# Kernel tuning notes

Hardware: AMD Instinct MI355X
Metric: run time of the kernel (lower is better)

The kernel has to match this reference:

```python
import jax, jax.numpy as jnp
import numpy as np

ALPHA = 0.95   # membrane decay
VTH = 1.0      # firing threshold
BN_EPS = 1e-5
SS_BETA = 10.0  # SuperSpike surrogate slope (used in bwd module)


def _spike(v):
    # Heaviside spike on (v - vth) already subtracted
    return (v > 0).astype(v.dtype)


def _batchnorm(h, scale, bias):
    # per-timestep batch norm over the batch axis (train mode, batch stats)
    mu = jnp.mean(h, axis=0, keepdims=True)
    var = jnp.mean(jnp.square(h - mu), axis=0, keepdims=True)
    return (h - mu) * jax.lax.rsqrt(var + BN_EPS) * scale + bias


def _lif_layer(x, W, scale=None, bias=None):
    # x: [T, B, F_in] -> spikes z: [T, B, F_out]
    T, B, _ = x.shape
    F_out = W.shape[1]
    I = jnp.einsum('tbf,fo->tbo', x, W)  # precompute dense projection for all steps

    def step(v, i_t):
        if scale is not None:
            i_t = _batchnorm(i_t, scale, bias)
        v = ALPHA * v + i_t
        z = _spike(v - VTH)
        v = v * (1.0 - z)  # reset-to-zero
        return v, z

    v0 = jnp.zeros((B, F_out), dtype=x.dtype)
    _, z = jax.lax.scan(step, v0, I)
    return z


def setup_inputs() -> dict:
    key = jax.random.key(0)
    k1, k2, k3 = jax.random.split(key, 3)
    B, T, H, Wd, C = 512, 100, 28, 28, 2
    inputs = jax.random.uniform(k1, (B, T, H, Wd, C), dtype=jnp.float32)
    trgt = jax.random.randint(k2, (B,), 0, 10)
    W1 = jax.random.normal(k3, (784, 100), dtype=jnp.float32) * (1.0 / np.sqrt(784))
    bn_scale = jnp.ones((100,), dtype=jnp.float32)
    bn_bias = jnp.zeros((100,), dtype=jnp.float32)
    W2 = jax.random.normal(jax.random.fold_in(key, 7), (100, 10), dtype=jnp.float32) * (1.0 / np.sqrt(100))
    return {"inputs": inputs, "trgt": trgt, "W1": W1, "bn_scale": bn_scale,
            "bn_bias": bn_bias, "W2": W2}


def reference(inputs, trgt, W1, bn_scale, bn_bias, W2):
    # inputs: [B, T, H, W, C]
    x = jnp.mean(inputs, axis=-1, keepdims=True)        # [B,T,H,W,1]
    x = jnp.swapaxes(x, 0, 1)                            # [T,B,H,W,1]
    x = jnp.reshape(x, (x.shape[0], x.shape[1], -1))     # [T,B,784]
    z1 = _lif_layer(x, W1, bn_scale, bn_bias)            # [T,B,100]
    z2 = _lif_layer(z1, W2)                              # [T,B,10]
    out = jnp.mean(z2, axis=0)                           # [B,10]
    return out
```

## Files before the change

### kernel.cpp

```cpp
#include <hip/hip_runtime.h>

#define T_STEPS 100
#define BATCH   512
#define FIN     784
#define O1      100
#define O2      10
#define KC1     28
#define NC1     (FIN / KC1)

typedef __attribute__((ext_vector_type(4))) double f64x4;

__global__ __launch_bounds__(64) void k0_probe(int* __restrict__ maps) {
  const int l = threadIdx.x;
  const f64x4 z = {0.0, 0.0, 0.0, 0.0};
  f64x4 pr = __builtin_amdgcn_mfma_f64_16x16x4f64((double)(l & 15), 0.25, z, 0, 0, 0);
  f64x4 pc = __builtin_amdgcn_mfma_f64_16x16x4f64(0.25, (double)(l & 15), z, 0, 0, 0);
#pragma unroll
  for (int r = 0; r < 4; ++r) {
    int rm = (int)(pr[r] + 0.5); rm = rm < 0 ? 0 : (rm > 15 ? 15 : rm);
    int cm = (int)(pc[r] + 0.5); cm = cm < 0 ? 0 : (cm > 15 ? 15 : cm);
    maps[l * 8 + r]     = rm;
    maps[l * 8 + 4 + r] = cm;
  }
}

__global__ __launch_bounds__(512, 6) void k1_mfma(const float* __restrict__ in,
                                                  const float* __restrict__ W1,
                                                  const int* __restrict__ maps,
                                                  double* __restrict__ I1T) {
  __shared__ double AI[KC1][66];
  __shared__ double WS[KC1][O1];
  const int tid = threadIdx.x;
  const int l   = tid & 63;
  const int w   = tid >> 6;
  const int wb  = w & 3;
  const int wo  = w >> 2;
  const int r16 = l & 15;
  const int q16 = l >> 4;
  const int b0  = (int)blockIdx.x * 64;
  const int t   = (int)blockIdx.y;

  const int4 rm = *reinterpret_cast<const int4*>(maps + l * 8);
  const int4 cm = *reinterpret_cast<const int4*>(maps + l * 8 + 4);

  bool iact[2]; int irow[2], iq[2]; const float* ibp[2];
#pragma unroll
  for (int p = 0; p < 2; ++p) {
    const int i = p * 512 + tid;
    iact[p] = (i < 896);
    irow[p] = iact[p] ? i / 14 : 0;
    iq[p]   = i - irow[p] * 14;
    ibp[p]  = in + ((size_t)(b0 + irow[p]) * T_STEPS + t) * (FIN * 2) + iq[p] * 4;
  }
  bool wact[3]; int wk[3], woh[3]; const float2* wbp[3];
#pragma unroll
  for (int p = 0; p < 3; ++p) {
    const int i = p * 512 + tid;
    wact[p] = (i < 1400);
    wk[p]   = wact[p] ? i / 50 : 0;
    woh[p]  = (i - wk[p] * 50) * 2;
    wbp[p]  = reinterpret_cast<const float2*>(W1) + ((size_t)wk[p] * O1 + woh[p]) / 2;
  }

  float4 ist[2];
  float2 wst[3];

#pragma unroll
  for (int p = 0; p < 2; ++p) if (iact[p]) ist[p] = *reinterpret_cast<const float4*>(ibp[p]);
#pragma unroll
  for (int p = 0; p < 3; ++p) if (wact[p]) wst[p] = wbp[p][0];

  f64x4 acc0 = {0.0, 0.0, 0.0, 0.0};
  f64x4 acc1 = {0.0, 0.0, 0.0, 0.0};
  f64x4 acc2 = {0.0, 0.0, 0.0, 0.0};
  f64x4 acc3 = {0.0, 0.0, 0.0, 0.0};

  for (int c = 0; c < NC1; ++c) {
    __syncthreads();
#pragma unroll
    for (int p = 0; p < 2; ++p)
      if (iact[p]) {
        AI[iq[p] * 2 + 0][irow[p]] = 0.5 * ((double)ist[p].x + (double)ist[p].y);
        AI[iq[p] * 2 + 1][irow[p]] = 0.5 * ((double)ist[p].z + (double)ist[p].w);
      }
#pragma unroll
    for (int p = 0; p < 3; ++p)
      if (wact[p]) {
        double2 wv; wv.x = (double)wst[p].x; wv.y = (double)wst[p].y;
        *reinterpret_cast<double2*>(&WS[wk[p]][woh[p]]) = wv;
      }
    if (c + 1 < NC1) {
#pragma unroll
      for (int p = 0; p < 2; ++p)
        if (iact[p]) ist[p] = *reinterpret_cast<const float4*>(ibp[p] + (c + 1) * 56);
#pragma unroll
      for (int p = 0; p < 3; ++p)
        if (wact[p]) wst[p] = wbp[p][(size_t)(c + 1) * (KC1 * O1 / 2)];
    }
    __syncthreads();
    if (wo == 0) {
#pragma unroll
      for (int q = 0; q < KC1 / 4; ++q) {
        const double bv = AI[q * 4 + q16][wb * 16 + r16];
        const double* wr = &WS[q * 4 + q16][r16];
        acc0 = __builtin_amdgcn_mfma_f64_16x16x4f64(wr[0],  bv, acc0, 0, 0, 0);
        acc1 = __builtin_amdgcn_mfma_f64_16x16x4f64(wr[16], bv, acc1, 0, 0, 0);
        acc2 = __builtin_amdgcn_mfma_f64_16x16x4f64(wr[32], bv, acc2, 0, 0, 0);
        acc3 = __builtin_amdgcn_mfma_f64_16x16x4f64(wr[48], bv, acc3, 0, 0, 0);
      }
    } else {
#pragma unroll
      for (int q = 0; q < KC1 / 4; ++q) {
        const double bv = AI[q * 4 + q16][wb * 16 + r16];
        const double* wr = &WS[q * 4 + q16][r16];
        acc0 = __builtin_amdgcn_mfma_f64_16x16x4f64(wr[64], bv, acc0, 0, 0, 0);
        acc1 = __builtin_amdgcn_mfma_f64_16x16x4f64(wr[80], bv, acc1, 0, 0, 0);
        acc2 = __builtin_amdgcn_mfma_f64_16x16x4f64(wr[84], bv, acc2, 0, 0, 0);
      }
    }
  }

  double* base = I1T + (size_t)t * O1 * BATCH + (b0 + wb * 16);
#define STORE_TILE(ACC, O0)                                          \
  {                                                                  \
    base[(size_t)((O0) + rm.x) * BATCH + cm.x] = (ACC)[0];           \
    base[(size_t)((O0) + rm.y) * BATCH + cm.y] = (ACC)[1];           \
    base[(size_t)((O0) + rm.z) * BATCH + cm.z] = (ACC)[2];           \
    base[(size_t)((O0) + rm.w) * BATCH + cm.w] = (ACC)[3];           \
  }
  if (wo == 0) {
    STORE_TILE(acc0, 0);
    STORE_TILE(acc1, 16);
    STORE_TILE(acc2, 32);
    STORE_TILE(acc3, 48);
  } else {
    STORE_TILE(acc0, 64);
    STORE_TILE(acc1, 80);
    STORE_TILE(acc2, 84);
  }
#undef STORE_TILE
}

__global__ __launch_bounds__(256) void k2_bnstats(const double* __restrict__ I1T,
                                                  double* __restrict__ mu,
                                                  double* __restrict__ rstd) {
  const int r    = blockIdx.x * 4 + (threadIdx.x >> 6);
  const int lane = threadIdx.x & 63;
  const double2* row2 = reinterpret_cast<const double2*>(I1T + (size_t)r * BATCH) + lane * 4;
  double v[8];
#pragma unroll
  for (int u = 0; u < 4; ++u) {
    double2 p = row2[u];
    v[2 * u] = p.x; v[2 * u + 1] = p.y;
  }
  double s = 0.0;
#pragma unroll
  for (int u = 0; u < 8; ++u) s += v[u];
#pragma unroll
  for (int m = 32; m >= 1; m >>= 1) s += __shfl_xor(s, m, 64);
  const double mean = s / 512.0;
  double q = 0.0;
#pragma unroll
  for (int u = 0; u < 8; ++u) { double d = v[u] - mean; q += d * d; }
#pragma unroll
  for (int m = 32; m >= 1; m >>= 1) q += __shfl_xor(q, m, 64);
  if (lane == 0) {
    mu[r]   = mean;
    rstd[r] = 1.0 / sqrt(q / 512.0 + 1e-5);
  }
}

__global__ __launch_bounds__(512) void k3_lif1(const double* __restrict__ I1T,
                                               const double* __restrict__ mu,
                                               const double* __restrict__ rstd,
                                               const float* __restrict__ scale,
                                               const float* __restrict__ bias,
                                               float* __restrict__ z1T) {
  const int o = blockIdx.x;
  const int b = threadIdx.x;
  const double sc = (double)scale[o], bs = (double)bias[o];
  double v = 0.0;
  for (int tc = 0; tc < T_STEPS; tc += 10) {
    double x[10], muv[10], rsv[10];
#pragma unroll
    for (int u = 0; u < 10; ++u) {
      const int t = tc + u;
      x[u]   = I1T[((size_t)t * O1 + o) * BATCH + b];
      muv[u] = mu[t * O1 + o];
      rsv[u] = rstd[t * O1 + o];
    }
#pragma unroll
    for (int u = 0; u < 10; ++u) {
      const double i = ((x[u] - muv[u]) * rsv[u]) * sc + bs;
      v = 0.95 * v + i;
      const bool z = (v > 1.0);
      z1T[((size_t)(tc + u) * O1 + o) * BATCH + b] = z ? 1.0f : 0.0f;
      if (z) v = 0.0;
    }
  }
}

__global__ __launch_bounds__(512) void k4_proj2(const float* __restrict__ z1T,
                                                const float* __restrict__ W2,
                                                double* __restrict__ I2) {
  __shared__ double W2_lds[O1 * O2];
  const int t = blockIdx.x;
  const int b = threadIdx.x;
  for (int i = threadIdx.x; i < O1 * O2; i += 512) W2_lds[i] = (double)W2[i];
  __syncthreads();
  double acc[O2];
#pragma unroll
  for (int j = 0; j < O2; ++j) acc[j] = 0.0;
  for (int o = 0; o < O1; ++o) {
    const double z = (double)z1T[((size_t)t * O1 + o) * BATCH + b];
#pragma unroll
    for (int j = 0; j < O2; ++j) acc[j] += z * W2_lds[o * O2 + j];
  }
#pragma unroll
  for (int j = 0; j < O2; ++j)
    I2[((size_t)t * O2 + j) * BATCH + b] = acc[j];
}

__global__ __launch_bounds__(512) void k5_lif2(const double* __restrict__ I2,
                                               float* __restrict__ out) {
  const int j = blockIdx.x;
  const int b = threadIdx.x;
  double v = 0.0;
  int cnt = 0;
  for (int tc = 0; tc < T_STEPS; tc += 10) {
    double x[10];
#pragma unroll
    for (int u = 0; u < 10; ++u)
      x[u] = I2[((size_t)(tc + u) * O2 + j) * BATCH + b];
#pragma unroll
    for (int u = 0; u < 10; ++u) {
      v = 0.95 * v + x[u];
      if (v > 1.0) { ++cnt; v = 0.0; }
    }
  }
  out[b * O2 + j] = (float)((double)cnt / 100.0);
}

extern "C" void kernel_launch(void* const* d_in, const int* in_sizes, int n_in,
                              void* d_out, int out_size, void* d_ws, size_t ws_size,
                              hipStream_t stream) {
  const float* in    = (const float*)d_in[0];
  const float* W1    = (const float*)d_in[2];
  const float* scale = (const float*)d_in[3];
  const float* bias  = (const float*)d_in[4];
  const float* W2    = (const float*)d_in[5];
  float* out = (float*)d_out;

  char* ws = (char*)d_ws;
  size_t off = 0;
  int*    maps = (int*)(ws + off);    off += 4096;
  double* I1T  = (double*)(ws + off); off += (size_t)T_STEPS * O1 * BATCH * sizeof(double);
  double* mu   = (double*)(ws + off); off += (size_t)T_STEPS * O1 * sizeof(double);
  double* rstd = (double*)(ws + off); off += (size_t)T_STEPS * O1 * sizeof(double);
  float*  z1T  = (float*)(ws + off);  off += (size_t)T_STEPS * O1 * BATCH * sizeof(float);
  double* I2   = (double*)(ws + off); off += (size_t)T_STEPS * O2 * BATCH * sizeof(double);

  k0_probe  <<<dim3(1), 64, 0, stream>>>(maps);
  k1_mfma   <<<dim3(BATCH / 64, T_STEPS), 512, 0, stream>>>(in, W1, maps, I1T);
  k2_bnstats<<<dim3(T_STEPS * O1 / 4), 256, 0, stream>>>(I1T, mu, rstd);
  k3_lif1   <<<dim3(O1), 512, 0, stream>>>(I1T, mu, rstd, scale, bias, z1T);
  k4_proj2  <<<dim3(T_STEPS), 512, 0, stream>>>(z1T, W2, I2);
  k5_lif2   <<<dim3(O2), 512, 0, stream>>>(I2, out);
}
```

Baseline: 256.8 us.

## Load W1 directly into registers, shrink k1 tiles, inline MFMA lane-map probe

The W1 shared-memory staging is removed. Each lane now loads the weight values its MFMA operands need straight from global memory (L2/L1 cached) into registers per chunk. The batch tile halves to 32 with 256-thread blocks, which doubles the grid, and the separate probe kernel that computed MFMA lane mappings is folded into k1 as per-lane MFMA calls. This cuts LDS traffic, syncs and one kernel launch, but adds uncached-pattern global weight loads that are issued synchronously each chunk rather than prefetched.

Result: slower. 266.8 us (+3.9%).

```diff
diff --git a/kernel.cpp b/kernel.cpp
--- a/kernel.cpp
+++ b/kernel.cpp
@@ -10,71 +10,51 @@
 
 typedef __attribute__((ext_vector_type(4))) double f64x4;
 
-__global__ __launch_bounds__(64) void k0_probe(int* __restrict__ maps) {
-  const int l = threadIdx.x;
-  const f64x4 z = {0.0, 0.0, 0.0, 0.0};
-  f64x4 pr = __builtin_amdgcn_mfma_f64_16x16x4f64((double)(l & 15), 0.25, z, 0, 0, 0);
-  f64x4 pc = __builtin_amdgcn_mfma_f64_16x16x4f64(0.25, (double)(l & 15), z, 0, 0, 0);
-#pragma unroll
-  for (int r = 0; r < 4; ++r) {
-    int rm = (int)(pr[r] + 0.5); rm = rm < 0 ? 0 : (rm > 15 ? 15 : rm);
-    int cm = (int)(pc[r] + 0.5); cm = cm < 0 ? 0 : (cm > 15 ? 15 : cm);
-    maps[l * 8 + r]     = rm;
-    maps[l * 8 + 4 + r] = cm;
-  }
-}
-
-__global__ __launch_bounds__(512, 6) void k1_mfma(const float* __restrict__ in,
+__global__ __launch_bounds__(256, 4) void k1_mfma(const float* __restrict__ in,
                                                   const float* __restrict__ W1,
-                                                  const int* __restrict__ maps,
                                                   double* __restrict__ I1T) {
-  __shared__ double AI[KC1][66];
-  __shared__ double WS[KC1][O1];
+  __shared__ double AI[KC1][34];
   const int tid = threadIdx.x;
   const int l   = tid & 63;
   const int w   = tid >> 6;
-  const int wb  = w & 3;
-  const int wo  = w >> 2;
+  const int wb  = w & 1;
+  const int wo  = w >> 1;
   const int r16 = l & 15;
   const int q16 = l >> 4;
-  const int b0  = (int)blockIdx.x * 64;
+  const int b0  = (int)blockIdx.x * 32;
   const int t   = (int)blockIdx.y;
 
-  const int4 rm = *reinterpret_cast<const int4*>(maps + l * 8);
-  const int4 cm = *reinterpret_cast<const int4*>(maps + l * 8 + 4);
-
   bool iact[2]; int irow[2], iq[2]; const float* ibp[2];
 #pragma unroll
   for (int p = 0; p < 2; ++p) {
-    const int i = p * 512 + tid;
-    iact[p] = (i < 896);
+    const int i = p * 256 + tid;
+    iact[p] = (i < 448);
     irow[p] = iact[p] ? i / 14 : 0;
     iq[p]   = i - irow[p] * 14;
     ibp[p]  = in + ((size_t)(b0 + irow[p]) * T_STEPS + t) * (FIN * 2) + iq[p] * 4;
   }
-  bool wact[3]; int wk[3], woh[3]; const float2* wbp[3];
-#pragma unroll
-  for (int p = 0; p < 3; ++p) {
-    const int i = p * 512 + tid;
-    wact[p] = (i < 1400);
-    wk[p]   = wact[p] ? i / 50 : 0;
-    woh[p]  = (i - wk[p] * 50) * 2;
-    wbp[p]  = reinterpret_cast<const float2*>(W1) + ((size_t)wk[p] * O1 + woh[p]) / 2;
-  }
 
   float4 ist[2];
-  float2 wst[3];
-
 #pragma unroll
   for (int p = 0; p < 2; ++p) if (iact[p]) ist[p] = *reinterpret_cast<const float4*>(ibp[p]);
-#pragma unroll
-  for (int p = 0; p < 3; ++p) if (wact[p]) wst[p] = wbp[p][0];
+
+  const f64x4 z = {0.0, 0.0, 0.0, 0.0};
+  f64x4 pr = __builtin_amdgcn_mfma_f64_16x16x4f64((double)r16, 0.25, z, 0, 0, 0);
+  f64x4 pc = __builtin_amdgcn_mfma_f64_16x16x4f64(0.25, (double)r16, z, 0, 0, 0);
+  int rmv[4], cmv[4];
+#pragma unroll
+  for (int r = 0; r < 4; ++r) {
+    int rm = (int)(pr[r] + 0.5); rmv[r] = rm < 0 ? 0 : (rm > 15 ? 15 : rm);
+    int cm = (int)(pc[r] + 0.5); cmv[r] = cm < 0 ? 0 : (cm > 15 ? 15 : cm);
+  }
 
   f64x4 acc0 = {0.0, 0.0, 0.0, 0.0};
   f64x4 acc1 = {0.0, 0.0, 0.0, 0.0};
   f64x4 acc2 = {0.0, 0.0, 0.0, 0.0};
   f64x4 acc3 = {0.0, 0.0, 0.0, 0.0};
 
+  const float* pW0 = W1 + (size_t)q16 * O1 + r16 + (wo ? 64 : 0);
+
   for (int c = 0; c < NC1; ++c) {
     __syncthreads();
 #pragma unroll
@@ -83,50 +63,57 @@
         AI[iq[p] * 2 + 0][irow[p]] = 0.5 * ((double)ist[p].x + (double)ist[p].y);
         AI[iq[p] * 2 + 1][irow[p]] = 0.5 * ((double)ist[p].z + (double)ist[p].w);
       }
-#pragma unroll
-    for (int p = 0; p < 3; ++p)
-      if (wact[p]) {
-        double2 wv; wv.x = (double)wst[p].x; wv.y = (double)wst[p].y;
-        *reinterpret_cast<double2*>(&WS[wk[p]][woh[p]]) = wv;
-      }
+    float wreg[7][4];
+    const float* pWc = pW0 + (size_t)c * (KC1 * O1);
+    if (wo == 0) {
+#pragma unroll
+      for (int q = 0; q < 7; ++q) {
+        wreg[q][0] = pWc[q * 400 +  0];
+        wreg[q][1] = pWc[q * 400 + 16];
+        wreg[q][2] = pWc[q * 400 + 32];
+        wreg[q][3] = pWc[q * 400 + 48];
+      }
+    } else {
+#pragma unroll
+      for (int q = 0; q < 7; ++q) {
+        wreg[q][0] = pWc[q * 400 +  0];
+        wreg[q][1] = pWc[q * 400 + 16];
+        wreg[q][2] = pWc[q * 400 + 20];
+      }
+    }
     if (c + 1 < NC1) {
 #pragma unroll
       for (int p = 0; p < 2; ++p)
         if (iact[p]) ist[p] = *reinterpret_cast<const float4*>(ibp[p] + (c + 1) * 56);
-#pragma unroll
-      for (int p = 0; p < 3; ++p)
-        if (wact[p]) wst[p] = wbp[p][(size_t)(c + 1) * (KC1 * O1 / 2)];
     }
     __syncthreads();
     if (wo == 0) {
 #pragma unroll
-      for (int q = 0; q < KC1 / 4; ++q) {
+      for (int q = 0; q < 7; ++q) {
         const double bv = AI[q * 4 + q16][wb * 16 + r16];
-        const double* wr = &WS[q * 4 + q16][r16];
-        acc0 = __builtin_amdgcn_mfma_f64_16x16x4f64(wr[0],  bv, acc0, 0, 0, 0);
-        acc1 = __builtin_amdgcn_mfma_f64_16x16x4f64(wr[16], bv, acc1, 0, 0, 0);
-        acc2 = __builtin_amdgcn_mfma_f64_16x16x4f64(wr[32], bv, acc2, 0, 0, 0);
-        acc3 = __builtin_amdgcn_mfma_f64_16x16x4f64(wr[48], bv, acc3, 0, 0, 0);
+        acc0 = __builtin_amdgcn_mfma_f64_16x16x4f64((double)wreg[q][0], bv, acc0, 0, 0, 0);
+        acc1 = __builtin_amdgcn_mfma_f64_16x16x4f64((double)wreg[q][1], bv, acc1, 0, 0, 0);
+        acc2 = __builtin_amdgcn_mfma_f64_16x16x4f64((double)wreg[q][2], bv, acc2, 0, 0, 0);
+        acc3 = __builtin_amdgcn_mfma_f64_16x16x4f64((double)wreg[q][3], bv, acc3, 0, 0, 0);
       }
     } else {
 #pragma unroll
-      for (int q = 0; q < KC1 / 4; ++q) {
+      for (int q = 0; q < 7; ++q) {
         const double bv = AI[q * 4 + q16][wb * 16 + r16];
-        const double* wr = &WS[q * 4 + q16][r16];
-        acc0 = __builtin_amdgcn_mfma_f64_16x16x4f64(wr[64], bv, acc0, 0, 0, 0);
-        acc1 = __builtin_amdgcn_mfma_f64_16x16x4f64(wr[80], bv, acc1, 0, 0, 0);
-        acc2 = __builtin_amdgcn_mfma_f64_16x16x4f64(wr[84], bv, acc2, 0, 0, 0);
+        acc0 = __builtin_amdgcn_mfma_f64_16x16x4f64((double)wreg[q][0], bv, acc0, 0, 0, 0);
+        acc1 = __builtin_amdgcn_mfma_f64_16x16x4f64((double)wreg[q][1], bv, acc1, 0, 0, 0);
+        acc2 = __builtin_amdgcn_mfma_f64_16x16x4f64((double)wreg[q][2], bv, acc2, 0, 0, 0);
       }
     }
   }
 
   double* base = I1T + (size_t)t * O1 * BATCH + (b0 + wb * 16);
-#define STORE_TILE(ACC, O0)                                          \
-  {                                                                  \
-    base[(size_t)((O0) + rm.x) * BATCH + cm.x] = (ACC)[0];           \
-    base[(size_t)((O0) + rm.y) * BATCH + cm.y] = (ACC)[1];           \
-    base[(size_t)((O0) + rm.z) * BATCH + cm.z] = (ACC)[2];           \
-    base[(size_t)((O0) + rm.w) * BATCH + cm.w] = (ACC)[3];           \
+#define STORE_TILE(ACC, O0)                                               \
+  {                                                                       \
+    base[(size_t)((O0) + rmv[0]) * BATCH + cmv[0]] = (ACC)[0];            \
+    base[(size_t)((O0) + rmv[1]) * BATCH + cmv[1]] = (ACC)[1];            \
+    base[(size_t)((O0) + rmv[2]) * BATCH + cmv[2]] = (ACC)[2];            \
+    base[(size_t)((O0) + rmv[3]) * BATCH + cmv[3]] = (ACC)[3];            \
   }
   if (wo == 0) {
     STORE_TILE(acc0, 0);
@@ -253,15 +240,13 @@
 
   char* ws = (char*)d_ws;
   size_t off = 0;
-  int*    maps = (int*)(ws + off);    off += 4096;
   double* I1T  = (double*)(ws + off); off += (size_t)T_STEPS * O1 * BATCH * sizeof(double);
   double* mu   = (double*)(ws + off); off += (size_t)T_STEPS * O1 * sizeof(double);
   double* rstd = (double*)(ws + off); off += (size_t)T_STEPS * O1 * sizeof(double);
   float*  z1T  = (float*)(ws + off);  off += (size_t)T_STEPS * O1 * BATCH * sizeof(float);
   double* I2   = (double*)(ws + off); off += (size_t)T_STEPS * O2 * BATCH * sizeof(double);
 
-  k0_probe  <<<dim3(1), 64, 0, stream>>>(maps);
-  k1_mfma   <<<dim3(BATCH / 64, T_STEPS), 512, 0, stream>>>(in, W1, maps, I1T);
+  k1_mfma   <<<dim3(BATCH / 32, T_STEPS), 256, 0, stream>>>(in, W1, I1T);
   k2_bnstats<<<dim3(T_STEPS * O1 / 4), 256, 0, stream>>>(I1T, mu, rstd);
   k3_lif1   <<<dim3(O1), 512, 0, stream>>>(I1T, mu, rstd, scale, bias, z1T);
   k4_proj2  <<<dim3(T_STEPS), 512, 0, stream>>>(z1T, W2, I2);
```
